# Kernel optimization log

Measured on AMD Instinct MI355X. Metric: run time of the kernel, lower is better.

The kernel has to match this reference:

```python
import jax, jax.numpy as jnp
import numpy as np
from jax import lax

C = 128
HEADS = 4
WS = 7      # spatial search window (per side radius 3)
WT = 1      # temporal radius -> frames t-1..t+1
EPS = 1e-6

_R = WS // 2
OFFS = np.array([(dt, dh, dw)
                 for dt in range(-WT, WT + 1)
                 for dh in range(-_R, _R + 1)
                 for dw in range(-_R, _R + 1)], dtype=np.int32)  # [L,3]


def layernorm_c(x, g, b):
    # LayerNorm2D: normalize over channel dim of [B,T,C,H,W]
    mu = jnp.mean(x, axis=2, keepdims=True)
    var = jnp.var(x, axis=2, keepdims=True)
    xn = (x - mu) * lax.rsqrt(var + EPS)
    return xn * g[None, None, :, None, None] + b[None, None, :, None, None]


def conv2d(x, w, b):
    y = lax.conv_general_dilated(x, w, (1, 1), 'SAME',
                                 dimension_numbers=('NCHW', 'OIHW', 'NCHW'))
    return y + b[None, :, None, None]


def setup_inputs() -> dict:
    key = jax.random.key(0)
    ks = jax.random.split(key, 16)
    B, T, H, W = 1, 4, 128, 128
    vid = jax.random.normal(ks[0], (B, T, C, H, W), jnp.float32)
    flows = jax.random.normal(ks[1], (B, T, 2, H, W), jnp.float32)
    s = 1.0 / np.sqrt(C)
    Wq = jax.random.normal(ks[2], (C, C), jnp.float32) * s
    Wk = jax.random.normal(ks[3], (C, C), jnp.float32) * s
    Wv = jax.random.normal(ks[4], (C, C), jnp.float32) * s
    Wo = jax.random.normal(ks[5], (C, C), jnp.float32) * s
    g0 = jnp.ones((C,), jnp.float32); b0 = jnp.zeros((C,), jnp.float32)
    g1 = jnp.ones((C,), jnp.float32); b1 = jnp.zeros((C,), jnp.float32)
    sc = 1.0 / np.sqrt(C * 9)
    w_r1 = jax.random.normal(ks[6], (C, C, 3, 3), jnp.float32) * sc
    b_r1 = jnp.zeros((C,), jnp.float32)
    w_r2 = jax.random.normal(ks[7], (C, C, 3, 3), jnp.float32) * sc
    b_r2 = jnp.zeros((C,), jnp.float32)
    return dict(vid=vid, flows=flows, g0=g0, b0=b0, Wq=Wq, Wk=Wk, Wv=Wv, Wo=Wo,
                g1=g1, b1=b1, w_r1=w_r1, b_r1=b_r1, w_r2=w_r2, b_r2=b_r2)


def _forward(vid, flows, g0, b0, Wq, Wk, Wv, Wo, g1, b1, w_r1, b_r1, w_r2, b_r2):
    B, T, _, H, W = vid.shape
    hd = C // HEADS
    N = T * H * W
    scale = hd ** -0.5

    x = layernorm_c(vid, g0, b0)
    q = jnp.einsum('btchw,oc->btohw', x, Wq)
    k = jnp.einsum('btchw,oc->btohw', x, Wk)
    v = jnp.einsum('btchw,oc->btohw', x, Wv)
    qh = q.transpose(0, 1, 3, 4, 2).reshape(B, N, HEADS, hd)
    kf = k.transpose(0, 1, 3, 4, 2).reshape(B, N, C)
    vf = v.transpose(0, 1, 3, 4, 2).reshape(B, N, C)

    tt = jnp.arange(T)[:, None, None]
    hh = jnp.arange(H)[None, :, None]
    ww = jnp.arange(W)[None, None, :]
    fh = flows[:, :, 0]  # [B,T,H,W]
    fw = flows[:, :, 1]
    offs = jnp.asarray(OFFS)

    def score_body(_, off):
        dt, dh, dw = off[0], off[1], off[2]
        t_i = jnp.clip(tt + dt, 0, T - 1)                        # [T,H,W]
        oh = jnp.round(fh * dt).astype(jnp.int32)                 # flow-guided center
        ow = jnp.round(fw * dt).astype(jnp.int32)
        h_i = jnp.clip(hh[None] + oh + dh, 0, H - 1)              # [B,T,H,W]
        w_i = jnp.clip(ww[None] + ow + dw, 0, W - 1)
        flat = ((jnp.broadcast_to(t_i[None], (B, T, H, W)) * H + h_i) * W + w_i).reshape(B, N)
        kg = jnp.take_along_axis(kf, flat[:, :, None], axis=1).reshape(B, N, HEADS, hd)
        s = jnp.einsum('bnhd,bnhd->bnh', qh, kg) * scale
        return None, (s, flat)

    _, (scores, flats) = lax.scan(score_body, None, offs)         # [L,B,N,HD], [L,B,N]
    wts = jax.nn.softmax(scores, axis=0)

    def agg_body(acc, inp):
        wl, fl = inp
        vg = jnp.take_along_axis(vf, fl[:, :, None], axis=1).reshape(B, N, HEADS, hd)
        return acc + wl[..., None] * vg, None

    acc, _ = lax.scan(agg_body, jnp.zeros((B, N, HEADS, hd), vid.dtype), (wts, flats))
    attn = acc.reshape(B, T, H, W, C).transpose(0, 1, 4, 2, 3)
    attn = jnp.einsum('btchw,oc->btohw', attn, Wo)

    vid1 = vid + attn
    y = layernorm_c(vid1, g1, b1)
    yb = y.reshape(B * T, C, H, W)
    r = conv2d(yb, w_r1, b_r1)
    r = jax.nn.gelu(r)
    r = conv2d(r, w_r2, b_r2)
    res = (yb + r).reshape(B, T, C, H, W)
    return vid1 + res


def reference(vid, flows, g0, b0, Wq, Wk, Wv, Wo, g1, b1, w_r1, b_r1, w_r2, b_r2):
    return _forward(vid, flows, g0, b0, Wq, Wk, Wv, Wo, g1, b1, w_r1, b_r1, w_r2, b_r2)
```

## Files before the change

### kernel.cpp

```cpp
#include <hip/hip_runtime.h>

__device__ __forceinline__ float bflo(unsigned int u){ return __builtin_bit_cast(float, (unsigned int)(u<<16)); }
__device__ __forceinline__ float bfhi(unsigned int u){ return __builtin_bit_cast(float, (unsigned int)(u & 0xffff0000u)); }
__device__ __forceinline__ float bfhiraw(unsigned int u){ return __builtin_bit_cast(float, u); }
__device__ __forceinline__ float b2f(unsigned short s){ return __builtin_bit_cast(float, ((unsigned int)s)<<16); }
__device__ __forceinline__ unsigned short f2b(float f){
  unsigned int x = __builtin_bit_cast(unsigned int, f);
  x += 0x7fffu + ((x>>16)&1u);
  return (unsigned short)(x>>16);
}
__device__ __forceinline__ unsigned int packbf(float a, float b){
  return (unsigned int)f2b(a) | ((unsigned int)f2b(b)<<16);
}
__device__ __forceinline__ float dpp_swap1(float s){
  int so = __builtin_amdgcn_mov_dpp(__builtin_bit_cast(int, s), 0xB1, 0xF, 0xF, true);
  return __builtin_bit_cast(float, so);
}

using bf16x8 = __attribute__((ext_vector_type(8))) short;
using f32x4  = __attribute__((ext_vector_type(4))) float;

#define NPOS 65536
#define SLOT_ELEMS 8388608

__global__ __launch_bounds__(256) void k_wprep(const float* __restrict__ w1,
                                               const float* __restrict__ w2,
                                               unsigned short* __restrict__ o1,
                                               unsigned short* __restrict__ o2){
  int idx = blockIdx.x*256 + threadIdx.x;
  if (idx >= 147456) return;
  int o = idx / 1152;
  int rem = idx - o*1152;
  int c = rem / 9;
  int tap = rem - c*9;
  int dsti = tap*16384 + o*128 + c;
  o1[dsti] = f2b(w1[idx]);
  o2[dsti] = f2b(w2[idx]);
}

__global__ __launch_bounds__(256) void k_ln_nchw(const float* __restrict__ vid,
                                                 const float* __restrict__ g,
                                                 const float* __restrict__ b,
                                                 unsigned short* __restrict__ xf){
  int n = blockIdx.x*256 + threadIdx.x;
  int t = n >> 14, hw = n & 16383;
  const float* base = vid + (size_t)t*2097152 + hw;
  float s=0.f, ss=0.f;
  #pragma unroll 8
  for (int c=0;c<128;c++){ float v=base[(size_t)c*16384]; s+=v; ss+=v*v; }
  float mu  = s*0.0078125f;
  float var = fmaxf(ss*0.0078125f - mu*mu, 0.f);
  float rs  = rsqrtf(var + 1e-6f);
  unsigned int* op = (unsigned int*)(xf + (size_t)n*128);
  #pragma unroll 4
  for (int c=0;c<128;c+=2){
    float v0=(base[(size_t)c*16384]    -mu)*rs*g[c]  +b[c];
    float v1=(base[(size_t)(c+1)*16384]-mu)*rs*g[c+1]+b[c+1];
    op[c>>1]=packbf(v0,v1);
  }
}

__global__ __launch_bounds__(256) void k_ln_rows(const unsigned short* __restrict__ x,
                                                 const float* __restrict__ g,
                                                 const float* __restrict__ b,
                                                 unsigned short* __restrict__ y){
  int n = blockIdx.x*256 + threadIdx.x;
  const unsigned int* p = (const unsigned int*)(x + (size_t)n*128);
  float s=0.f, ss=0.f;
  #pragma unroll 8
  for (int j=0;j<64;j++){ unsigned int u=p[j]; float v0=bflo(u),v1=bfhi(u); s+=v0+v1; ss+=v0*v0+v1*v1; }
  float mu  = s*0.0078125f;
  float var = fmaxf(ss*0.0078125f - mu*mu, 0.f);
  float rs  = rsqrtf(var + 1e-6f);
  unsigned int* op=(unsigned int*)(y+(size_t)n*128);
  #pragma unroll 8
  for (int j=0;j<64;j++){
    unsigned int u=p[j];
    float v0=(bflo(u)-mu)*rs*g[2*j]  +b[2*j];
    float v1=(bfhi(u)-mu)*rs*g[2*j+1]+b[2*j+1];
    op[j]=packbf(v0,v1);
  }
}

__global__ __launch_bounds__(256) void k_qkv(const unsigned short* xf,
                                             const float* __restrict__ Wq,
                                             const float* __restrict__ Wk,
                                             const float* __restrict__ Wv,
                                             unsigned short* qf,
                                             unsigned short* __restrict__ kfo,
                                             unsigned short* __restrict__ vfo){
  __shared__ unsigned short wlds[16384];
  int wave = threadIdx.x>>6, lane = threadIdx.x&63;
  int m0 = blockIdx.x*64 + wave*16;
  int mrow = lane&15, quad = lane>>4;
  bf16x8 a[4];
  const unsigned short* ap = xf + (size_t)(m0+mrow)*128 + quad*8;
  #pragma unroll
  for (int kc=0;kc<4;kc++) a[kc] = *(const bf16x8*)(ap + kc*32);
  const float* Ws[3] = {Wq, Wk, Wv};
  unsigned short* outs[3] = {qf, kfo, vfo};
  for (int mat=0; mat<3; mat++){
    __syncthreads();
    { const float2* src=(const float2*)Ws[mat]; unsigned int* dst=(unsigned int*)wlds;
      for (int i=threadIdx.x;i<8192;i+=256){ float2 wv=src[i]; dst[i]=packbf(wv.x,wv.y); } }
    __syncthreads();
    unsigned short* out = outs[mat];
    for (int nt=0;nt<8;nt++){
      f32x4 acc = {0.f,0.f,0.f,0.f};
      #pragma unroll
      for (int kc=0;kc<4;kc++){
        bf16x8 bfr = *(const bf16x8*)(wlds + (nt*16+mrow)*128 + kc*32 + quad*8);
        acc = __builtin_amdgcn_mfma_f32_16x16x32_bf16(a[kc], bfr, acc, 0,0,0);
      }
      int col = nt*16+mrow;
      unsigned short* op = out + (size_t)(m0 + quad*4)*128 + col;
      #pragma unroll
      for (int r=0;r<4;r++) op[(size_t)r*128] = f2b(acc[r]);
    }
  }
}

__global__ __launch_bounds__(256) void k_attn(const unsigned short* qf,
                                              const unsigned short* __restrict__ kf,
                                              const unsigned short* __restrict__ vf,
                                              const float* __restrict__ flw,
                                              unsigned short* attf){
  int xcd = blockIdx.x & 7;
  int j   = blockIdx.x >> 3;
  int t       = j >> 6;
  int r       = j & 63;
  int h_local = r >> 2;
  int wq      = r & 3;
  int h = xcd*16 + h_local;
  int w = wq*32 + (threadIdx.x >> 3);
  int head  = (threadIdx.x >> 1) & 3;
  int cpart = threadIdx.x & 1;
  int hw = (h<<7) + w;
  int n  = (t<<14) + hw;
  float fh = flw[t*32768 + hw];
  float fw = flw[t*32768 + 16384 + hw];
  unsigned coff = head*32 + cpart*16;
  const uint4* qp = (const uint4*)(qf + (size_t)n*128 + coff);
  float q[16];
  #pragma unroll
  for (int i=0;i<2;i++){
    uint4 qv = qp[i];
    q[8*i+0]=bflo(qv.x); q[8*i+1]=bfhi(qv.x);
    q[8*i+2]=bflo(qv.y); q[8*i+3]=bfhi(qv.y);
    q[8*i+4]=bflo(qv.z); q[8*i+5]=bfhi(qv.z);
    q[8*i+6]=bflo(qv.w); q[8*i+7]=bfhi(qv.w);
  }
  #pragma unroll
  for (int i=0;i<16;i++) q[i] *= 0.17677669529663687f;
  float acc[16];
  #pragma unroll
  for (int i=0;i<16;i++) acc[i]=0.f;
  float l = 0.f;
  #pragma unroll 1
  for (int dt=-1; dt<=1; dt++){
    int ti = t+dt; ti = ti<0?0:(ti>3?3:ti);
    int oh = (int)rintf(fh*(float)dt);
    int ow = (int)rintf(fw*(float)dt);
    int hb = h+oh, wb = w+ow;
    #pragma unroll 1
    for (int dh=-3; dh<=3; dh++){
      int hi = hb+dh; hi = hi<0?0:(hi>127?127:hi);
      int rb = (ti<<14)+(hi<<7);
      int wm3 = wb-3;
      int w0c = wm3<0?0:(wm3>127?127:wm3);
      unsigned bo0 = ((unsigned)(rb+w0c)<<7) + coff;
      uint4 ka0 = ((const uint4*)(kf + bo0))[0];
      uint4 ka1 = ((const uint4*)(kf + bo0))[1];
      uint4 va0 = ((const uint4*)(vf + bo0))[0];
      uint4 va1 = ((const uint4*)(vf + bo0))[1];
      #pragma unroll
      for (int i=0;i<7;i++){
        uint4 kb0, kb1, vb0, vb1;
        if (i<6){
          int wi = wm3+i+1; wi = wi<0?0:(wi>127?127:wi);
          unsigned bon = ((unsigned)(rb+wi)<<7) + coff;
          kb0 = ((const uint4*)(kf + bon))[0];
          kb1 = ((const uint4*)(kf + bon))[1];
          vb0 = ((const uint4*)(vf + bon))[0];
          vb1 = ((const uint4*)(vf + bon))[1];
        }
        float s = 0.f;
        s += q[0]*bflo(ka0.x) + q[1]*bfhiraw(ka0.x);
        s += q[2]*bflo(ka0.y) + q[3]*bfhiraw(ka0.y);
        s += q[4]*bflo(ka0.z) + q[5]*bfhiraw(ka0.z);
        s += q[6]*bflo(ka0.w) + q[7]*bfhiraw(ka0.w);
        s += q[8]*bflo(ka1.x) + q[9]*bfhiraw(ka1.x);
        s += q[10]*bflo(ka1.y) + q[11]*bfhiraw(ka1.y);
        s += q[12]*bflo(ka1.z) + q[13]*bfhiraw(ka1.z);
        s += q[14]*bflo(ka1.w) + q[15]*bfhiraw(ka1.w);
        s += dpp_swap1(s);
        float e = __expf(s);
        l += e;
        acc[0]  += e*bflo(va0.x); acc[1]  += e*bfhiraw(va0.x);
        acc[2]  += e*bflo(va0.y); acc[3]  += e*bfhiraw(va0.y);
        acc[4]  += e*bflo(va0.z); acc[5]  += e*bfhiraw(va0.z);
        acc[6]  += e*bflo(va0.w); acc[7]  += e*bfhiraw(va0.w);
        acc[8]  += e*bflo(va1.x); acc[9]  += e*bfhiraw(va1.x);
        acc[10] += e*bflo(va1.y); acc[11] += e*bfhiraw(va1.y);
        acc[12] += e*bflo(va1.z); acc[13] += e*bfhiraw(va1.z);
        acc[14] += e*bflo(va1.w); acc[15] += e*bfhiraw(va1.w);
        ka0=kb0; ka1=kb1; va0=vb0; va1=vb1;
      }
    }
  }
  float inv = 1.f/l;
  unsigned int* op = (unsigned int*)(attf + (size_t)n*128 + coff);
  #pragma unroll
  for (int i=0;i<8;i++) op[i]=packbf(acc[2*i]*inv, acc[2*i+1]*inv);
}

__global__ __launch_bounds__(256) void k_wo(const unsigned short* attf,
                                            const float* __restrict__ Wo,
                                            const float* __restrict__ vid,
                                            unsigned short* vid1){
  __shared__ unsigned short wlds[16384];
  int wave = threadIdx.x>>6, lane = threadIdx.x&63;
  int m0 = blockIdx.x*64 + wave*16;
  int mrow = lane&15, quad = lane>>4;
  bf16x8 a[4];
  const unsigned short* ap = attf + (size_t)(m0+mrow)*128 + quad*8;
  #pragma unroll
  for (int kc=0;kc<4;kc++) a[kc] = *(const bf16x8*)(ap + kc*32);
  { const float2* src=(const float2*)Wo; unsigned int* dst=(unsigned int*)wlds;
    for (int i=threadIdx.x;i<8192;i+=256){ float2 wv=src[i]; dst[i]=packbf(wv.x,wv.y); } }
  __syncthreads();
  for (int nt=0;nt<8;nt++){
    f32x4 acc={0.f,0.f,0.f,0.f};
    #pragma unroll
    for (int kc=0;kc<4;kc++){
      bf16x8 bfr = *(const bf16x8*)(wlds + (nt*16+mrow)*128 + kc*32 + quad*8);
      acc = __builtin_amdgcn_mfma_f32_16x16x32_bf16(a[kc], bfr, acc, 0,0,0);
    }
    int col = nt*16+mrow;
    #pragma unroll
    for (int r=0;r<4;r++){
      int nrow = m0 + quad*4 + r;
      int tt = nrow>>14, hww = nrow&16383;
      float resid = vid[(size_t)tt*2097152 + (size_t)col*16384 + hww];
      vid1[(size_t)nrow*128 + col] = f2b(resid + acc[r]);
    }
  }
}

#define CONV_PROLOG \
  __shared__ unsigned short wlds[8192]; \
  int wv = threadIdx.x>>6, lane = threadIdx.x&63; \
  int mrow = lane&15, quad = lane>>4; \
  int chalf = blockIdx.x & 1; \
  int h = (blockIdx.x>>1) & 127; \
  int frame = blockIdx.x>>8; \
  size_t nf = (size_t)frame*16384; \
  f32x4 accA[4], accB[4]; \
  _Pragma("unroll") \
  for (int i=0;i<4;i++){ accA[i]=(f32x4){0.f,0.f,0.f,0.f}; accB[i]=(f32x4){0.f,0.f,0.f,0.f}; } \
  { const uint4* sp=(const uint4*)(wtap + chalf*8192); \
    uint4 s0=sp[threadIdx.x], s1=sp[threadIdx.x+256], s2=sp[threadIdx.x+512], s3=sp[threadIdx.x+768]; \
    uint4* d4=(uint4*)wlds; \
    d4[threadIdx.x]=s0; d4[threadIdx.x+256]=s1; d4[threadIdx.x+512]=s2; d4[threadIdx.x+768]=s3; } \
  __syncthreads(); \
  _Pragma("unroll 1") \
  for (int tap=0; tap<9; tap++){ \
    uint4 s0,s1,s2,s3; \
    if (tap<8){ const uint4* sp=(const uint4*)(wtap + (size_t)(tap+1)*16384 + chalf*8192); \
      s0=sp[threadIdx.x]; s1=sp[threadIdx.x+256]; s2=sp[threadIdx.x+512]; s3=sp[threadIdx.x+768]; } \
    int ky=tap/3, kx=tap-3*ky; \
    int h2=h+ky-1; \
    if ((unsigned)h2<128u){ \
      int wA = wv*32 + mrow + kx - 1;             \
      int wAc = wA < 0 ? 0 : wA; \
      int wB = wA + 16;                           \
      int wBc = wB > 127 ? 127 : wB; \
      const unsigned short* rowp = src + (nf + (size_t)h2*128)*128 + quad*8; \
      const unsigned short* apA = rowp + (size_t)wAc*128; \
      const unsigned short* apB = rowp + (size_t)wBc*128; \
      bf16x8 aA[4], aB[4]; \
      _Pragma("unroll") \
      for (int kc=0;kc<4;kc++){ aA[kc]=*(const bf16x8*)(apA+kc*32); aB[kc]=*(const bf16x8*)(apB+kc*32); } \
      if (kx==0 && wv==0 && mrow==0){ _Pragma("unroll") for (int kc=0;kc<4;kc++) aA[kc]=(bf16x8){0,0,0,0,0,0,0,0}; } \
      if (kx==2 && wv==3 && mrow==15){ _Pragma("unroll") for (int kc=0;kc<4;kc++) aB[kc]=(bf16x8){0,0,0,0,0,0,0,0}; } \
      _Pragma("unroll") \
      for (int nt=0;nt<4;nt++){ \
        _Pragma("unroll") \
        for (int kc=0;kc<4;kc++){ \
          bf16x8 bfr=*(const bf16x8*)(wlds + (nt*16+mrow)*128 + kc*32 + quad*8); \
          accA[nt]=__builtin_amdgcn_mfma_f32_16x16x32_bf16(aA[kc],bfr,accA[nt],0,0,0); \
          accB[nt]=__builtin_amdgcn_mfma_f32_16x16x32_bf16(aB[kc],bfr,accB[nt],0,0,0); \
        } \
      } \
    } \
    __syncthreads(); \
    if (tap<8){ uint4* d4=(uint4*)wlds; \
      d4[threadIdx.x]=s0; d4[threadIdx.x+256]=s1; d4[threadIdx.x+512]=s2; d4[threadIdx.x+768]=s3; \
      __syncthreads(); } \
  }

__global__ __launch_bounds__(256) void k_conv_gelu(const unsigned short* __restrict__ src,
                                                   const unsigned short* __restrict__ wtap,
                                                   const float* __restrict__ bias,
                                                   unsigned short* __restrict__ dst){
  CONV_PROLOG
  #pragma unroll
  for (int nt=0;nt<4;nt++){
    int col = chalf*64 + nt*16 + mrow;
    float bb = bias[col];
    #pragma unroll
    for (int r=0;r<4;r++){
      int pA = h*128 + wv*32 + quad*4 + r;
      float xA = accA[nt][r]+bb;
      float zA = 0.7978845608028654f*(xA+0.044715f*xA*xA*xA);
      dst[(nf+(size_t)pA)*128+col] = f2b(xA * __builtin_amdgcn_rcpf(1.f + __expf(-2.f*zA)));
      float xB = accB[nt][r]+bb;
      float zB = 0.7978845608028654f*(xB+0.044715f*xB*xB*xB);
      dst[(nf+(size_t)(pA+16))*128+col] = f2b(xB * __builtin_amdgcn_rcpf(1.f + __expf(-2.f*zB)));
    }
  }
}

__global__ __launch_bounds__(256) void k_conv_final(const unsigned short* __restrict__ src,
                                                    const unsigned short* __restrict__ wtap,
                                                    const float* __restrict__ bias,
                                                    const unsigned short* __restrict__ yb,
                                                    const unsigned short* __restrict__ vid1,
                                                    float* __restrict__ out){
  CONV_PROLOG
  #pragma unroll
  for (int nt=0;nt<4;nt++){
    int col = chalf*64 + nt*16 + mrow;
    float bb = bias[col];
    #pragma unroll
    for (int r=0;r<4;r++){
      int pA = h*128 + wv*32 + quad*4 + r;
      size_t rowA = nf+(size_t)pA, rowB = rowA+16;
      float xA = accA[nt][r]+bb;
      out[(size_t)frame*2097152 + (size_t)col*16384 + pA] =
        b2f(vid1[rowA*128+col]) + b2f(yb[rowA*128+col]) + xA;
      float xB = accB[nt][r]+bb;
      out[(size_t)frame*2097152 + (size_t)col*16384 + pA + 16] =
        b2f(vid1[rowB*128+col]) + b2f(yb[rowB*128+col]) + xB;
    }
  }
}

extern "C" void kernel_launch(void* const* d_in, const int* in_sizes, int n_in,
                              void* d_out, int out_size, void* d_ws, size_t ws_size,
                              hipStream_t stream) {
  const float* vid  = (const float*)d_in[0];
  const float* flw  = (const float*)d_in[1];
  const float* g0   = (const float*)d_in[2];
  const float* b0   = (const float*)d_in[3];
  const float* Wq   = (const float*)d_in[4];
  const float* Wk   = (const float*)d_in[5];
  const float* Wv   = (const float*)d_in[6];
  const float* Wo   = (const float*)d_in[7];
  const float* g1   = (const float*)d_in[8];
  const float* b1   = (const float*)d_in[9];
  const float* wr1  = (const float*)d_in[10];
  const float* br1  = (const float*)d_in[11];
  const float* wr2  = (const float*)d_in[12];
  const float* br2  = (const float*)d_in[13];
  float* out = (float*)d_out;

  unsigned short* A  = (unsigned short*)d_ws;
  unsigned short* Bs = A + SLOT_ELEMS;
  unsigned short* Cs = Bs + SLOT_ELEMS;
  bool four = ws_size >= (size_t)4*SLOT_ELEMS*2 + 2*294912;
  unsigned short* D  = four ? (Cs + SLOT_ELEMS) : A;
  unsigned short* wt1 = Cs + SLOT_ELEMS + (four ? SLOT_ELEMS : 0);
  unsigned short* wt2 = wt1 + 147456;

  k_wprep   <<<576, 256, 0, stream>>>(wr1, wr2, wt1, wt2);
  k_ln_nchw <<<256, 256, 0, stream>>>(vid, g0, b0, A);
  k_qkv     <<<1024,256, 0, stream>>>(A, Wq, Wk, Wv, D, Bs, Cs);
  k_attn    <<<2048,256, 0, stream>>>(D, Bs, Cs, flw, D);
  k_wo      <<<1024,256, 0, stream>>>(D, Wo, vid, D);
  k_ln_rows <<<256, 256, 0, stream>>>(D, g1, b1, Bs);
  k_conv_gelu <<<1024,256,0, stream>>>(Bs, wt1, br1, Cs);
  k_conv_final<<<1024,256,0, stream>>>(Cs, wt2, br2, Bs, D, out);
}
```

Baseline: 468.0 us.

## Store QKV as fp16 in head-interleaved layout; one thread per head in attention

```diff
diff --git a/kernel.cpp b/kernel.cpp
--- a/kernel.cpp
+++ b/kernel.cpp
@@ -2,7 +2,6 @@
 
 __device__ __forceinline__ float bflo(unsigned int u){ return __builtin_bit_cast(float, (unsigned int)(u<<16)); }
 __device__ __forceinline__ float bfhi(unsigned int u){ return __builtin_bit_cast(float, (unsigned int)(u & 0xffff0000u)); }
-__device__ __forceinline__ float bfhiraw(unsigned int u){ return __builtin_bit_cast(float, u); }
 __device__ __forceinline__ float b2f(unsigned short s){ return __builtin_bit_cast(float, ((unsigned int)s)<<16); }
 __device__ __forceinline__ unsigned short f2b(float f){
   unsigned int x = __builtin_bit_cast(unsigned int, f);
@@ -12,13 +11,24 @@
 __device__ __forceinline__ unsigned int packbf(float a, float b){
   return (unsigned int)f2b(a) | ((unsigned int)f2b(b)<<16);
 }
-__device__ __forceinline__ float dpp_swap1(float s){
-  int so = __builtin_amdgcn_mov_dpp(__builtin_bit_cast(int, s), 0xB1, 0xF, 0xF, true);
-  return __builtin_bit_cast(float, so);
-}
 
 using bf16x8 = __attribute__((ext_vector_type(8))) short;
 using f32x4  = __attribute__((ext_vector_type(4))) float;
+using h2     = __attribute__((ext_vector_type(2))) _Float16;
+
+__device__ __forceinline__ unsigned short f2h(float f){
+  return __builtin_bit_cast(unsigned short, (_Float16)f);
+}
+__device__ __forceinline__ void qkstep(float& s, h2 qq, unsigned int ku){
+  h2 kk = __builtin_bit_cast(h2, ku);
+  s += (float)qq.x * (float)kk.x;
+  s += (float)qq.y * (float)kk.y;
+}
+__device__ __forceinline__ void pvstep(float& a0, float& a1, float e, unsigned int vu){
+  h2 vv = __builtin_bit_cast(h2, vu);
+  a0 += e * (float)vv.x;
+  a1 += e * (float)vv.y;
+}
 
 #define NPOS 65536
 #define SLOT_ELEMS 8388608
@@ -105,6 +115,7 @@
       for (int i=threadIdx.x;i<8192;i+=256){ float2 wv=src[i]; dst[i]=packbf(wv.x,wv.y); } }
     __syncthreads();
     unsigned short* out = outs[mat];
+    float m = (mat==0) ? 0.17677669529663687f : 1.0f;
     for (int nt=0;nt<8;nt++){
       f32x4 acc = {0.f,0.f,0.f,0.f};
       #pragma unroll
@@ -113,14 +124,15 @@
         acc = __builtin_amdgcn_mfma_f32_16x16x32_bf16(a[kc], bfr, acc, 0,0,0);
       }
       int col = nt*16+mrow;
-      unsigned short* op = out + (size_t)(m0 + quad*4)*128 + col;
+      int pos = ((col&24)<<2) | ((col>>5)<<3) | (col&7);
+      unsigned short* op = out + (size_t)(m0 + quad*4)*128 + pos;
       #pragma unroll
-      for (int r=0;r<4;r++) op[(size_t)r*128] = f2b(acc[r]);
-    }
-  }
-}
-
-__global__ __launch_bounds__(256) void k_attn(const unsigned short* qf,
+      for (int r=0;r<4;r++) op[(size_t)r*128] = f2h(acc[r]*m);
+    }
+  }
+}
+
+__global__ __launch_bounds__(128) void k_attn(const unsigned short* qf,
                                               const unsigned short* __restrict__ kf,
                                               const unsigned short* __restrict__ vf,
                                               const float* __restrict__ flw,
@@ -132,29 +144,28 @@
   int h_local = r >> 2;
   int wq      = r & 3;
   int h = xcd*16 + h_local;
-  int w = wq*32 + (threadIdx.x >> 3);
-  int head  = (threadIdx.x >> 1) & 3;
-  int cpart = threadIdx.x & 1;
+  int w = wq*32 + (threadIdx.x >> 2);
+  int head  = threadIdx.x & 3;
   int hw = (h<<7) + w;
   int n  = (t<<14) + hw;
   float fh = flw[t*32768 + hw];
   float fw = flw[t*32768 + 16384 + hw];
-  unsigned coff = head*32 + cpart*16;
-  const uint4* qp = (const uint4*)(qf + (size_t)n*128 + coff);
-  float q[16];
-  #pragma unroll
-  for (int i=0;i<2;i++){
-    uint4 qv = qp[i];
-    q[8*i+0]=bflo(qv.x); q[8*i+1]=bfhi(qv.x);
-    q[8*i+2]=bflo(qv.y); q[8*i+3]=bfhi(qv.y);
-    q[8*i+4]=bflo(qv.z); q[8*i+5]=bfhi(qv.z);
-    q[8*i+6]=bflo(qv.w); q[8*i+7]=bfhi(qv.w);
-  }
-  #pragma unroll
-  for (int i=0;i<16;i++) q[i] *= 0.17677669529663687f;
-  float acc[16];
-  #pragma unroll
-  for (int i=0;i<16;i++) acc[i]=0.f;
+  unsigned hoff = head*8;
+  const unsigned short* kfh = kf + hoff;
+  const unsigned short* vfh = vf + hoff;
+  const uint4* qp = (const uint4*)(qf + (size_t)n*128 + hoff);
+  h2 q[16];
+  #pragma unroll
+  for (int i=0;i<4;i++){
+    uint4 qv = qp[4*i];
+    q[4*i+0]=__builtin_bit_cast(h2,qv.x);
+    q[4*i+1]=__builtin_bit_cast(h2,qv.y);
+    q[4*i+2]=__builtin_bit_cast(h2,qv.z);
+    q[4*i+3]=__builtin_bit_cast(h2,qv.w);
+  }
+  float acc[32];
+  #pragma unroll
+  for (int i=0;i<32;i++) acc[i]=0.f;
   float l = 0.f;
   #pragma unroll 1
   for (int dt=-1; dt<=1; dt++){
@@ -168,50 +179,46 @@
       int rb = (ti<<14)+(hi<<7);
       int wm3 = wb-3;
       int w0c = wm3<0?0:(wm3>127?127:wm3);
-      unsigned bo0 = ((unsigned)(rb+w0c)<<7) + coff;
-      uint4 ka0 = ((const uint4*)(kf + bo0))[0];
-      uint4 ka1 = ((const uint4*)(kf + bo0))[1];
-      uint4 va0 = ((const uint4*)(vf + bo0))[0];
-      uint4 va1 = ((const uint4*)(vf + bo0))[1];
+      unsigned bo0 = (unsigned)(rb+w0c)<<7;
+      const uint4* kp = (const uint4*)(kfh + bo0);
+      const uint4* vp = (const uint4*)(vfh + bo0);
+      uint4 ka[4], va[4];
+      #pragma unroll
+      for (int c=0;c<4;c++){ ka[c]=kp[4*c]; va[c]=vp[4*c]; }
       #pragma unroll
       for (int i=0;i<7;i++){
-        uint4 kb0, kb1, vb0, vb1;
+        uint4 kb[4], vb[4];
         if (i<6){
           int wi = wm3+i+1; wi = wi<0?0:(wi>127?127:wi);
-          unsigned bon = ((unsigned)(rb+wi)<<7) + coff;
-          kb0 = ((const uint4*)(kf + bon))[0];
-          kb1 = ((const uint4*)(kf + bon))[1];
-          vb0 = ((const uint4*)(vf + bon))[0];
-          vb1 = ((const uint4*)(vf + bon))[1];
+          unsigned bon = (unsigned)(rb+wi)<<7;
+          const uint4* kp2 = (const uint4*)(kfh + bon);
+          const uint4* vp2 = (const uint4*)(vfh + bon);
+          #pragma unroll
+          for (int c=0;c<4;c++){ kb[c]=kp2[4*c]; vb[c]=vp2[4*c]; }
         }
-        float s = 0.f;
-        s += q[0]*bflo(ka0.x) + q[1]*bfhiraw(ka0.x);
-        s += q[2]*bflo(ka0.y) + q[3]*bfhiraw(ka0.y);
-        s += q[4]*bflo(ka0.z) + q[5]*bfhiraw(ka0.z);
-        s += q[6]*bflo(ka0.w) + q[7]*bfhiraw(ka0.w);
-        s += q[8]*bflo(ka1.x) + q[9]*bfhiraw(ka1.x);
-        s += q[10]*bflo(ka1.y) + q[11]*bfhiraw(ka1.y);
-        s += q[12]*bflo(ka1.z) + q[13]*bfhiraw(ka1.z);
-        s += q[14]*bflo(ka1.w) + q[15]*bfhiraw(ka1.w);
-        s += dpp_swap1(s);
-        float e = __expf(s);
+        float s0=0.f, s1=0.f, s2=0.f, s3=0.f;
+        qkstep(s0,q[0] ,ka[0].x); qkstep(s0,q[1] ,ka[0].y); qkstep(s0,q[2] ,ka[0].z); qkstep(s0,q[3] ,ka[0].w);
+        qkstep(s1,q[4] ,ka[1].x); qkstep(s1,q[5] ,ka[1].y); qkstep(s1,q[6] ,ka[1].z); qkstep(s1,q[7] ,ka[1].w);
+        qkstep(s2,q[8] ,ka[2].x); qkstep(s2,q[9] ,ka[2].y); qkstep(s2,q[10],ka[2].z); qkstep(s2,q[11],ka[2].w);
+        qkstep(s3,q[12],ka[3].x); qkstep(s3,q[13],ka[3].y); qkstep(s3,q[14],ka[3].z); qkstep(s3,q[15],ka[3].w);
+        float e = __expf((s0+s1)+(s2+s3));
         l += e;
-        acc[0]  += e*bflo(va0.x); acc[1]  += e*bfhiraw(va0.x);
-        acc[2]  += e*bflo(va0.y); acc[3]  += e*bfhiraw(va0.y);
-        acc[4]  += e*bflo(va0.z); acc[5]  += e*bfhiraw(va0.z);
-        acc[6]  += e*bflo(va0.w); acc[7]  += e*bfhiraw(va0.w);
-        acc[8]  += e*bflo(va1.x); acc[9]  += e*bfhiraw(va1.x);
-        acc[10] += e*bflo(va1.y); acc[11] += e*bfhiraw(va1.y);
-        acc[12] += e*bflo(va1.z); acc[13] += e*bfhiraw(va1.z);
-        acc[14] += e*bflo(va1.w); acc[15] += e*bfhiraw(va1.w);
-        ka0=kb0; ka1=kb1; va0=vb0; va1=vb1;
+        #pragma unroll
+        for (int c=0;c<4;c++){
+          pvstep(acc[8*c+0],acc[8*c+1],e,va[c].x);
+          pvstep(acc[8*c+2],acc[8*c+3],e,va[c].y);
+          pvstep(acc[8*c+4],acc[8*c+5],e,va[c].z);
+          pvstep(acc[8*c+6],acc[8*c+7],e,va[c].w);
+        }
+        #pragma unroll
+        for (int c=0;c<4;c++){ ka[c]=kb[c]; va[c]=vb[c]; }
       }
     }
   }
   float inv = 1.f/l;
-  unsigned int* op = (unsigned int*)(attf + (size_t)n*128 + coff);
-  #pragma unroll
-  for (int i=0;i<8;i++) op[i]=packbf(acc[2*i]*inv, acc[2*i+1]*inv);
+  unsigned int* op = (unsigned int*)(attf + (size_t)n*128 + head*32);
+  #pragma unroll
+  for (int i=0;i<16;i++) op[i]=packbf(acc[2*i]*inv, acc[2*i+1]*inv);
 }
 
 __global__ __launch_bounds__(256) void k_wo(const unsigned short* attf,
@@ -269,13 +276,13 @@
     if (tap<8){ const uint4* sp=(const uint4*)(wtap + (size_t)(tap+1)*16384 + chalf*8192); \
       s0=sp[threadIdx.x]; s1=sp[threadIdx.x+256]; s2=sp[threadIdx.x+512]; s3=sp[threadIdx.x+768]; } \
     int ky=tap/3, kx=tap-3*ky; \
-    int h2=h+ky-1; \
-    if ((unsigned)h2<128u){ \
+    int h2c=h+ky-1; \
+    if ((unsigned)h2c<128u){ \
       int wA = wv*32 + mrow + kx - 1;             \
       int wAc = wA < 0 ? 0 : wA; \
       int wB = wA + 16;                           \
       int wBc = wB > 127 ? 127 : wB; \
-      const unsigned short* rowp = src + (nf + (size_t)h2*128)*128 + quad*8; \
+      const unsigned short* rowp = src + (nf + (size_t)h2c*128)*128 + quad*8; \
       const unsigned short* apA = rowp + (size_t)wAc*128; \
       const unsigned short* apB = rowp + (size_t)wBc*128; \
       bf16x8 aA[4], aB[4]; \
@@ -376,7 +383,7 @@
   k_wprep   <<<576, 256, 0, stream>>>(wr1, wr2, wt1, wt2);
   k_ln_nchw <<<256, 256, 0, stream>>>(vid, g0, b0, A);
   k_qkv     <<<1024,256, 0, stream>>>(A, Wq, Wk, Wv, D, Bs, Cs);
-  k_attn    <<<2048,256, 0, stream>>>(D, Bs, Cs, flw, D);
+  k_attn    <<<2048,128, 0, stream>>>(D, Bs, Cs, flw, D);
   k_wo      <<<1024,256, 0, stream>>>(D, Wo, vid, D);
   k_ln_rows <<<256, 256, 0, stream>>>(D, g1, b1, Bs);
   k_conv_gelu <<<1024,256,0, stream>>>(Bs, wt1, br1, Cs);
```

New measurement: 486.8 us. 1.04x slower.
